# Performance work log

Measured on AMD Instinct MI355X. Metric: run time of the kernel, lower is better.

Reference implementation:

```python
import jax, jax.numpy as jnp
import numpy as np
from jax import lax

B, CIN, H, W = 2, 512, 64, 64
NCLS = 5
CI = CIN // 4      # inter_channels = 128
CQ = CI // 8       # PAM query/key channels = 16
EPS = 1e-5


def setup_inputs() -> dict:
    key = jax.random.key(0)
    it = iter(jax.random.split(key, 48))

    def nrm(shape, s=0.05):
        return jax.random.normal(next(it), shape, jnp.float32) * s

    def bn(c):
        w = jax.random.uniform(next(it), (c,), jnp.float32, 0.5, 1.5)
        b = nrm((c,))
        m = nrm((c,))
        v = jax.random.uniform(next(it), (c,), jnp.float32, 0.5, 1.5)
        return w, b, m, v

    inp = {}
    inp['x'] = jax.random.normal(next(it), (B, CIN, H, W), jnp.float32)
    inp['bn_a_w'], inp['bn_a_b'], inp['bn_a_m'], inp['bn_a_v'] = bn(CIN)
    inp['conv_a_w'] = nrm((CI, CIN, 3, 3))
    inp['bn_c_w'], inp['bn_c_b'], inp['bn_c_m'], inp['bn_c_v'] = bn(CIN)
    inp['conv_c_w'] = nrm((CI, CIN, 3, 3))
    inp['pam_q_w'] = nrm((CQ, CI)); inp['pam_q_b'] = nrm((CQ,))
    inp['pam_k_w'] = nrm((CQ, CI)); inp['pam_k_b'] = nrm((CQ,))
    inp['pam_v_w'] = nrm((CI, CI)); inp['pam_v_b'] = nrm((CI,))
    inp['pam_gamma'] = nrm((1,), 0.5)
    inp['cam_gamma'] = nrm((1,), 0.5)
    inp['bn_a1_w'], inp['bn_a1_b'], inp['bn_a1_m'], inp['bn_a1_v'] = bn(CI)
    inp['conv_a1_w'] = nrm((CIN, CI)); inp['conv_a1_b'] = nrm((CIN,))
    inp['bn_c1_w'], inp['bn_c1_b'], inp['bn_c1_m'], inp['bn_c1_v'] = bn(CI)
    inp['conv_c1_w'] = nrm((CIN, CI)); inp['conv_c1_b'] = nrm((CIN,))
    inp['out_a_w'] = nrm((NCLS, CIN)); inp['out_a_b'] = nrm((NCLS,))
    inp['out_c_w'] = nrm((NCLS, CIN)); inp['out_c_b'] = nrm((NCLS,))
    inp['out_f_w'] = nrm((NCLS, CIN)); inp['out_f_b'] = nrm((NCLS,))
    return inp


def _bn_relu(x, w, b, m, v):
    # eval-mode BatchNorm2d followed by ReLU
    scale = (w / jnp.sqrt(v + EPS))[None, :, None, None]
    shift = (b - m * w / jnp.sqrt(v + EPS))[None, :, None, None]
    return jax.nn.relu(x * scale + shift)


def _conv3(x, w):
    return lax.conv_general_dilated(x, w, (1, 1), 'SAME',
                                    dimension_numbers=('NCHW', 'OIHW', 'NCHW'))


def _conv1(x, w, b):
    # 1x1 conv as channel matmul
    return jnp.einsum('oi,bihw->bohw', w, x) + b[None, :, None, None]


def _pam(x, wq, bq, wk, bk, wv, bv, gamma):
    Bc, C, Hh, Ww = x.shape
    N = Hh * Ww
    q = _conv1(x, wq, bq).reshape(Bc, -1, N)   # [B,CQ,N]
    k = _conv1(x, wk, bk).reshape(Bc, -1, N)   # [B,CQ,N]
    v = _conv1(x, wv, bv).reshape(Bc, C, N)    # [B,C,N]
    energy = jnp.einsum('bcn,bcm->bnm', q, k)  # [B,N,N]
    attn = jax.nn.softmax(energy, axis=-1)
    out = jnp.einsum('bcm,bnm->bcn', v, attn).reshape(Bc, C, Hh, Ww)
    return gamma * out + x


def _cam(x, gamma):
    Bc, C, Hh, Ww = x.shape
    N = Hh * Ww
    f = x.reshape(Bc, C, N)
    energy = jnp.einsum('bcn,bdn->bcd', f, f)                    # [B,C,C]
    energy_new = jnp.max(energy, -1, keepdims=True) - energy
    attn = jax.nn.softmax(energy_new, axis=-1)
    out = jnp.einsum('bcd,bdn->bcn', attn, f).reshape(Bc, C, Hh, Ww)
    return gamma * out + x


def reference(x, bn_a_w, bn_a_b, bn_a_m, bn_a_v, conv_a_w,
              bn_c_w, bn_c_b, bn_c_m, bn_c_v, conv_c_w,
              pam_q_w, pam_q_b, pam_k_w, pam_k_b, pam_v_w, pam_v_b,
              pam_gamma, cam_gamma,
              bn_a1_w, bn_a1_b, bn_a1_m, bn_a1_v, conv_a1_w, conv_a1_b,
              bn_c1_w, bn_c1_b, bn_c1_m, bn_c1_v, conv_c1_w, conv_c1_b,
              out_a_w, out_a_b, out_c_w, out_c_b, out_f_w, out_f_b):
    # position-attention branch
    sa = _conv3(_bn_relu(x, bn_a_w, bn_a_b, bn_a_m, bn_a_v), conv_a_w)
    sa = _pam(sa, pam_q_w, pam_q_b, pam_k_w, pam_k_b, pam_v_w, pam_v_b, pam_gamma)
    sa = _conv1(_bn_relu(sa, bn_a1_w, bn_a1_b, bn_a1_m, bn_a1_v), conv_a1_w, conv_a1_b)
    # channel-attention branch
    sc = _conv3(_bn_relu(x, bn_c_w, bn_c_b, bn_c_m, bn_c_v), conv_c_w)
    sc = _cam(sc, cam_gamma)
    sc = _conv1(_bn_relu(sc, bn_c1_w, bn_c1_b, bn_c1_m, bn_c1_v), conv_c1_w, conv_c1_b)
    feat_fusion = sa + sc
    # dropout is identity at eval time
    sa_out = _conv1(sa, out_a_w, out_a_b)
    sc_out = _conv1(sc, out_c_w, out_c_b)
    sasc_out = _conv1(feat_fusion, out_f_w, out_f_b)
    return (feat_fusion, sasc_out, sa_out, sc_out)
```

## Files before the change

kernel.cpp:

```cpp
#include <hip/hip_runtime.h>

using u16 = unsigned short;
using short8 = __attribute__((ext_vector_type(8))) short;
using f32x4 = __attribute__((ext_vector_type(4))) float;

struct alignas(8) U16x4 { u16 x, y, z, w; };

__device__ __forceinline__ float bf2f(u16 u) {
  return __uint_as_float(((unsigned int)u) << 16);
}
__device__ __forceinline__ u16 f2bf(float f) {
  unsigned int u = __float_as_uint(f);
  unsigned int r = u + 0x7FFFu + ((u >> 16) & 1u);
  return (u16)(r >> 16);
}

__global__ void k_prep_w(const float* __restrict__ wa, const float* __restrict__ wc,
                         u16* __restrict__ Wb) {
  int idx = blockIdx.x * 256 + threadIdx.x;
  int j = idx & 7;
  int l = (idx >> 3) & 63;
  int ks = (idx >> 9) & 3;
  int rest = idx >> 11;
  int tap = rest % 9;
  int rest2 = rest / 9;
  int chunk = rest2 & 3;
  int mt = (rest2 >> 2) & 7;
  int br = rest2 >> 5;
  int co = mt * 16 + (l & 15);
  int ci = chunk * 128 + ks * 32 + (l >> 4) * 8 + j;
  const float* w = br ? wc : wa;
  Wb[idx] = f2bf(w[co * 4608 + ci * 9 + tap]);
}

__global__ void k_prep_w1(const float* __restrict__ wa, const float* __restrict__ wc,
                          u16* __restrict__ W1b) {
  int idx = blockIdx.x * 256 + threadIdx.x;
  int j = idx & 7;
  int l = (idx >> 3) & 63;
  int ks = (idx >> 9) & 3;
  int cot = (idx >> 11) & 31;
  int br = idx >> 16;
  int co = cot * 16 + (l & 15);
  int ci = ks * 32 + (l >> 4) * 8 + j;
  const float* w = br ? wc : wa;
  W1b[idx] = f2bf(w[co * 128 + ci]);
}

__global__ void k_prep_wqkv(const float* __restrict__ wq, const float* __restrict__ wk,
                            const float* __restrict__ wv, u16* __restrict__ Wq) {
  int idx = blockIdx.x * 256 + threadIdx.x;
  if (idx >= 20480) return;
  int j = idx & 7;
  int l = (idx >> 3) & 63;
  int ks = (idx >> 9) & 3;
  int cot = idx >> 11;
  int co = cot * 16 + (l & 15);
  int ci = ks * 32 + (l >> 4) * 8 + j;
  float w = co < 16 ? wq[co * 128 + ci]
          : (co < 32 ? wk[(co - 16) * 128 + ci] : wv[(co - 32) * 128 + ci]);
  Wq[idx] = f2bf(w);
}

__global__ __launch_bounds__(256) void k_bnrelu2t(const float* __restrict__ x,
    const float* __restrict__ wa, const float* __restrict__ ba,
    const float* __restrict__ ma, const float* __restrict__ va,
    const float* __restrict__ wc, const float* __restrict__ bc,
    const float* __restrict__ mc, const float* __restrict__ vc,
    u16* __restrict__ xa16, u16* __restrict__ xcb16) {
  __shared__ float sA[512], bA[512], sC[512], bC[512];
  __shared__ u16 ta[64 * 136], tc[64 * 136];
  int t = threadIdx.x;
  int h = blockIdx.x, b = blockIdx.y;
  for (int c = t; c < 512; c += 256) {
    float s1 = wa[c] * rsqrtf(va[c] + 1e-5f);
    sA[c] = s1; bA[c] = ba[c] - ma[c] * s1;
    float s2 = wc[c] * rsqrtf(vc[c] + 1e-5f);
    sC[c] = s2; bC[c] = bc[c] - mc[c] * s2;
  }
  __syncthreads();
  const float* xb = x + ((size_t)b << 21) + (h << 6);
  u16* oa = xa16 + ((size_t)b << 21) + ((size_t)h << 15);
  u16* oc = xcb16 + ((size_t)b << 21) + ((size_t)h << 15);
  int w = t & 63, cg = t >> 6;
  for (int c0 = 0; c0 < 512; c0 += 128) {
#pragma unroll
    for (int i = 0; i < 8; ++i) {
      int cl = cg * 4 + i * 16;
      int c = c0 + cl;
      const float* xp = xb + (size_t)c * 4096 + w;
      float v0 = xp[0], v1 = xp[4096], v2 = xp[8192], v3 = xp[12288];
      U16x4 pa, pc;
      pa.x = f2bf(fmaxf(fmaf(v0, sA[c], bA[c]), 0.f));
      pa.y = f2bf(fmaxf(fmaf(v1, sA[c + 1], bA[c + 1]), 0.f));
      pa.z = f2bf(fmaxf(fmaf(v2, sA[c + 2], bA[c + 2]), 0.f));
      pa.w = f2bf(fmaxf(fmaf(v3, sA[c + 3], bA[c + 3]), 0.f));
      pc.x = f2bf(fmaxf(fmaf(v0, sC[c], bC[c]), 0.f));
      pc.y = f2bf(fmaxf(fmaf(v1, sC[c + 1], bC[c + 1]), 0.f));
      pc.z = f2bf(fmaxf(fmaf(v2, sC[c + 2], bC[c + 2]), 0.f));
      pc.w = f2bf(fmaxf(fmaf(v3, sC[c + 3], bC[c + 3]), 0.f));
      *(U16x4*)(ta + w * 136 + cl) = pa;
      *(U16x4*)(tc + w * 136 + cl) = pc;
    }
    __syncthreads();
#pragma unroll
    for (int i = 0; i < 4; ++i) {
      int idx = t + i * 256;
      int ww = idx >> 4, c8 = (idx & 15) << 3;
      *(short8*)(oa + (size_t)ww * 512 + c0 + c8) = *(const short8*)(ta + ww * 136 + c8);
      *(short8*)(oc + (size_t)ww * 512 + c0 + c8) = *(const short8*)(tc + ww * 136 + c8);
    }
    __syncthreads();
  }
}

__global__ __launch_bounds__(256, 2) void k_conv3n(
    const u16* __restrict__ xa16, const u16* __restrict__ xcb16,
    const u16* __restrict__ Wb,
    float* __restrict__ sa0, float* __restrict__ sc0,
    u16* __restrict__ sa_nhwc, u16* __restrict__ sc16h, u16* __restrict__ sc16l) {
  __shared__ u16 xs[3 * 66 * 136];
  int t = threadIdx.x;
  int h = blockIdx.x;
  int z = blockIdx.y; int b = z & 1, br = z >> 1;
  int cosplit = blockIdx.z;
  const u16* xb = (br ? xcb16 : xa16) + ((size_t)b << 21);
  const u16* wb = Wb + (size_t)br * 589824;
  float* out = (br ? sc0 : sa0) + (((size_t)b * 128) << 12) + (h << 6);

  int lane = t & 63, wave = t >> 6;
  int mi = lane & 15, quad = lane >> 4;
  int mt = cosplit * 4 + wave;

  if (t < 96) {
    int dh = t >> 5, side = (t >> 4) & 1, c8 = t & 15;
    short8 z8 = {0, 0, 0, 0, 0, 0, 0, 0};
    *(short8*)(xs + (dh * 66 + side * 65) * 136 + c8 * 8) = z8;
  }

  f32x4 acc[4] = {};

  const u16* wlane = wb + lane * 8;
  const u16* bbase0 = xs + mi * 136 + quad * 8;

  for (int chunk = 0; chunk < 4; ++chunk) {
    int ci0 = chunk << 7;
    __syncthreads();
#pragma unroll
    for (int dh = 0; dh < 3; ++dh) {
      int hh = h + dh - 1;
      bool val = (hh >= 0) && (hh < 64);
      const u16* src = xb + (((size_t)hh << 6) << 9) + ci0;
#pragma unroll
      for (int i = 0; i < 4; ++i) {
        int idx = t + i * 256;
        int w = idx >> 4, c8 = (idx & 15) << 3;
        short8 v = {0, 0, 0, 0, 0, 0, 0, 0};
        if (val) v = *(const short8*)(src + ((size_t)w << 9) + c8);
        *(short8*)(xs + (dh * 66 + 1 + w) * 136 + c8) = v;
      }
    }
    __syncthreads();
    const u16* wchunk = wlane + (size_t)(mt * 4 + chunk) * 18432;
    short8 wreg[2][4];
#pragma unroll
    for (int ks = 0; ks < 4; ++ks)
      wreg[0][ks] = *(const short8*)(wchunk + ks * 512);
#pragma unroll
    for (int tap = 0; tap < 9; ++tap) {
      const int cb = tap & 1;
      if (tap < 8) {
        const u16* wn = wchunk + (tap + 1) * 2048;
#pragma unroll
        for (int ks = 0; ks < 4; ++ks)
          wreg[cb ^ 1][ks] = *(const short8*)(wn + ks * 512);
      }
      const int dh = tap / 3, dw = tap % 3;
      const u16* bp = bbase0 + (dh * 66 + dw) * 136;
#pragma unroll
      for (int ks = 0; ks < 4; ++ks) {
        short8 a = wreg[cb][ks];
#pragma unroll
        for (int nt = 0; nt < 4; ++nt) {
          short8 bf = *(const short8*)(bp + nt * 2176 + ks * 32);
          acc[nt] = __builtin_amdgcn_mfma_f32_16x16x32_bf16(a, bf, acc[nt], 0, 0, 0);
        }
      }
    }
  }
#pragma unroll
  for (int nt = 0; nt < 4; ++nt)
#pragma unroll
    for (int r = 0; r < 4; ++r) {
      int co = mt * 16 + quad * 4 + r;
      out[((size_t)co << 12) + nt * 16 + mi] = acc[nt][r];
    }
  if (br == 0) {
    u16* dstq = sa_nhwc + ((size_t)b << 19) + ((size_t)h << 6) * 128;
#pragma unroll
    for (int nt = 0; nt < 4; ++nt) {
      U16x4 v4;
      v4.x = f2bf(acc[nt][0]); v4.y = f2bf(acc[nt][1]);
      v4.z = f2bf(acc[nt][2]); v4.w = f2bf(acc[nt][3]);
      *(U16x4*)(dstq + (size_t)(nt * 16 + mi) * 128 + mt * 16 + quad * 4) = v4;
    }
  } else {
    u16* dh_ = sc16h + ((size_t)b << 19) + (h << 6);
    u16* dl_ = sc16l + ((size_t)b << 19) + (h << 6);
#pragma unroll
    for (int nt = 0; nt < 4; ++nt)
#pragma unroll
      for (int r = 0; r < 4; ++r) {
        int co = mt * 16 + quad * 4 + r;
        float xv = acc[nt][r];
        u16 hi = f2bf(xv);
        float lo = xv - bf2f(hi);
        size_t o = ((size_t)co << 12) + nt * 16 + mi;
        dh_[o] = hi;
        dl_[o] = f2bf(lo);
      }
  }
}

__global__ __launch_bounds__(256) void k_qkv(
    const u16* __restrict__ sa_nhwc, const u16* __restrict__ Wqkvb,
    const float* __restrict__ bq, const float* __restrict__ bk,
    const float* __restrict__ bv,
    float* __restrict__ qb, u16* __restrict__ k16t, u16* __restrict__ vt16) {
  __shared__ float bs[160];
  int t = threadIdx.x;
  int b = blockIdx.y, n0 = blockIdx.x * 128;
  if (t < 160) bs[t] = t < 16 ? bq[t] : (t < 32 ? bk[t - 16] : bv[t - 32]);
  __syncthreads();
  int lane = t & 63, wave = t >> 6;
  int mi = lane & 15, quad = lane >> 4;
  const u16* xb = sa_nhwc + ((size_t)b << 19) + (size_t)n0 * 128;
  const u16* wb = Wqkvb + lane * 8;
  f32x4 acc[2][10] = {};
  short8 bf[2][4];
#pragma unroll
  for (int ns = 0; ns < 2; ++ns) {
    int n = wave * 32 + ns * 16 + mi;
#pragma unroll
    for (int ks = 0; ks < 4; ++ks)
      bf[ns][ks] = *(const short8*)(xb + (size_t)n * 128 + ks * 32 + quad * 8);
  }
#pragma unroll
  for (int cot = 0; cot < 10; ++cot) {
    short8 a0 = *(const short8*)(wb + (size_t)(cot * 4 + 0) * 512);
    short8 a1 = *(const short8*)(wb + (size_t)(cot * 4 + 1) * 512);
    short8 a2 = *(const short8*)(wb + (size_t)(cot * 4 + 2) * 512);
    short8 a3 = *(const short8*)(wb + (size_t)(cot * 4 + 3) * 512);
#pragma unroll
    for (int ns = 0; ns < 2; ++ns) {
      acc[ns][cot] = __builtin_amdgcn_mfma_f32_16x16x32_bf16(a0, bf[ns][0], acc[ns][cot], 0, 0, 0);
      acc[ns][cot] = __builtin_amdgcn_mfma_f32_16x16x32_bf16(a1, bf[ns][1], acc[ns][cot], 0, 0, 0);
      acc[ns][cot] = __builtin_amdgcn_mfma_f32_16x16x32_bf16(a2, bf[ns][2], acc[ns][cot], 0, 0, 0);
      acc[ns][cot] = __builtin_amdgcn_mfma_f32_16x16x32_bf16(a3, bf[ns][3], acc[ns][cot], 0, 0, 0);
    }
  }
#pragma unroll
  for (int cot = 0; cot < 10; ++cot)
#pragma unroll
    for (int ns = 0; ns < 2; ++ns) {
      int n = n0 + wave * 32 + ns * 16 + mi;
      if (cot == 1) {
        u16 hv[4], lv[4];
#pragma unroll
        for (int r = 0; r < 4; ++r) {
          float v = acc[ns][1][r] + bs[16 + quad * 4 + r];
          u16 hi = f2bf(v);
          hv[r] = hi;
          lv[r] = f2bf(v - bf2f(hi));
        }
        u16* kd = k16t + (((size_t)b << 12) + n) * 32;
        U16x4 h4{hv[0], hv[1], hv[2], hv[3]};
        U16x4 l4{lv[0], lv[1], lv[2], lv[3]};
        *(U16x4*)(kd + quad * 4) = h4;
        *(U16x4*)(kd + 16 + quad * 4) = l4;
      } else {
#pragma unroll
        for (int r = 0; r < 4; ++r) {
          int co = cot * 16 + quad * 4 + r;
          float v = acc[ns][cot][r] + bs[co];
          if (co < 16) qb[((b * 16 + co) << 12) + n] = v;
          else vt16[((size_t)(b * 128 + co - 32) << 12) + n] = f2bf(v);
        }
      }
    }
}

__global__ __launch_bounds__(512, 4) void k_pam_pv(const float* __restrict__ qb,
    const u16* __restrict__ k16t, const u16* __restrict__ vt16,
    float* __restrict__ pvpart, float* __restrict__ pmax, float* __restrict__ psum) {
  constexpr int PSTR = 264;
  __shared__ u16 pL[32 * PSTR];
  __shared__ u16 qfh[32 * 16], qfl[32 * 16];
  __shared__ float wmx[8][2][16];
  __shared__ float wsm[8][2][16];
  int t = threadIdx.x;
  int b = blockIdx.y, n0 = blockIdx.x * 32;
  int mbeg = blockIdx.z << 11;
  int lane = t & 63, wave = t >> 6;
  int mi = lane & 15, quad = lane >> 4;
  int c0 = wave * 16;
  {
    int ch = t & 15, nl = t >> 4;
    float qv = qb[((size_t)(b * 16 + ch) << 12) + n0 + nl];
    u16 hi = f2bf(qv);
    qfh[nl * 16 + ch] = hi;
    qfl[nl * 16 + ch] = f2bf(qv - bf2f(hi));
  }
  const u16* kp = k16t + (((size_t)b << 12) + mbeg) * 32;
  const u16* vb = vt16 + ((size_t)b * 128 << 12);
  f32x4 acc[2] = {};
  float mr0 = -1e30f, mr1 = -1e30f, ssum0 = 0.f, ssum1 = 0.f;
  __syncthreads();
  int qoff = (quad & 1) * 8;
  short8 bq1[2], bq2[2];
  bq1[0] = *(const short8*)(qfh + mi * 16 + qoff);
  bq1[1] = *(const short8*)(qfh + (16 + mi) * 16 + qoff);
  bq2[0] = *(const short8*)(qfl + mi * 16 + qoff);
  bq2[1] = *(const short8*)(qfl + (16 + mi) * 16 + qoff);
  size_t abase = (size_t)(wave * 32 + mi) * 32 + quad * 8;
  short8 a0c = *(const short8*)(kp + abase);
  short8 a1c = *(const short8*)(kp + abase + 512);
  for (int it = 0; it < 8; ++it) {
    int m0r = it << 8;
    short8 vreg[8];
#pragma unroll
    for (int ksl = 0; ksl < 8; ++ksl)
      vreg[ksl] = *(const short8*)(vb + ((size_t)(c0 + mi) << 12) + mbeg + m0r + ksl * 32 + quad * 8);
    short8 a0n, a1n;
    if (it < 7) {
      a0n = *(const short8*)(kp + (size_t)(it + 1) * 8192 + abase);
      a1n = *(const short8*)(kp + (size_t)(it + 1) * 8192 + abase + 512);
    }
    f32x4 e00 = {}, e01 = {}, e10 = {}, e11 = {};
    e00 = __builtin_amdgcn_mfma_f32_16x16x32_bf16(a0c, bq1[0], e00, 0, 0, 0);
    e00 = __builtin_amdgcn_mfma_f32_16x16x32_bf16(a0c, bq2[0], e00, 0, 0, 0);
    e01 = __builtin_amdgcn_mfma_f32_16x16x32_bf16(a0c, bq1[1], e01, 0, 0, 0);
    e01 = __builtin_amdgcn_mfma_f32_16x16x32_bf16(a0c, bq2[1], e01, 0, 0, 0);
    e10 = __builtin_amdgcn_mfma_f32_16x16x32_bf16(a1c, bq1[0], e10, 0, 0, 0);
    e10 = __builtin_amdgcn_mfma_f32_16x16x32_bf16(a1c, bq2[0], e10, 0, 0, 0);
    e11 = __builtin_amdgcn_mfma_f32_16x16x32_bf16(a1c, bq1[1], e11, 0, 0, 0);
    e11 = __builtin_amdgcn_mfma_f32_16x16x32_bf16(a1c, bq2[1], e11, 0, 0, 0);
    float lm0 = fmaxf(fmaxf(fmaxf(e00[0], e00[1]), fmaxf(e00[2], e00[3])),
                      fmaxf(fmaxf(e10[0], e10[1]), fmaxf(e10[2], e10[3])));
    float lm1 = fmaxf(fmaxf(fmaxf(e01[0], e01[1]), fmaxf(e01[2], e01[3])),
                      fmaxf(fmaxf(e11[0], e11[1]), fmaxf(e11[2], e11[3])));
    lm0 = fmaxf(lm0, __shfl_xor(lm0, 16)); lm0 = fmaxf(lm0, __shfl_xor(lm0, 32));
    lm1 = fmaxf(lm1, __shfl_xor(lm1, 16)); lm1 = fmaxf(lm1, __shfl_xor(lm1, 32));
    if (quad == 0) { wmx[wave][0][mi] = lm0; wmx[wave][1][mi] = lm1; }
    __syncthreads();
    float cm0 = wmx[0][0][mi], cm1 = wmx[0][1][mi];
#pragma unroll
    for (int w = 1; w < 8; ++w) {
      cm0 = fmaxf(cm0, wmx[w][0][mi]);
      cm1 = fmaxf(cm1, wmx[w][1][mi]);
    }
    float mn0 = fmaxf(mr0, cm0), mn1 = fmaxf(mr1, cm1);
    float rs0 = __expf(mr0 - mn0), rs1 = __expf(mr1 - mn1);
#pragma unroll
    for (int r = 0; r < 4; ++r) { acc[0][r] *= rs0; acc[1][r] *= rs1; }
    float p00[4], p10[4], p01[4], p11[4];
    float ls0 = 0.f, ls1 = 0.f;
#pragma unroll
    for (int j = 0; j < 4; ++j) {
      p00[j] = __expf(e00[j] - mn0); p10[j] = __expf(e10[j] - mn0);
      p01[j] = __expf(e01[j] - mn1); p11[j] = __expf(e11[j] - mn1);
      ls0 += p00[j] + p10[j];
      ls1 += p01[j] + p11[j];
    }
    ssum0 = ssum0 * rs0 + ls0;
    ssum1 = ssum1 * rs1 + ls1;
    mr0 = mn0; mr1 = mn1;
    u16* prow0 = pL + mi * PSTR + wave * 32 + quad * 4;
    u16* prow1 = pL + (16 + mi) * PSTR + wave * 32 + quad * 4;
    U16x4 p;
    p.x = f2bf(p00[0]); p.y = f2bf(p00[1]); p.z = f2bf(p00[2]); p.w = f2bf(p00[3]);
    *(U16x4*)(prow0) = p;
    p.x = f2bf(p10[0]); p.y = f2bf(p10[1]); p.z = f2bf(p10[2]); p.w = f2bf(p10[3]);
    *(U16x4*)(prow0 + 16) = p;
    p.x = f2bf(p01[0]); p.y = f2bf(p01[1]); p.z = f2bf(p01[2]); p.w = f2bf(p01[3]);
    *(U16x4*)(prow1) = p;
    p.x = f2bf(p11[0]); p.y = f2bf(p11[1]); p.z = f2bf(p11[2]); p.w = f2bf(p11[3]);
    *(U16x4*)(prow1 + 16) = p;
    __syncthreads();
#pragma unroll
    for (int ksl = 0; ksl < 8; ++ksl) {
      const u16* pb0 = pL + mi * PSTR + ksl * 32 + quad * 8;
      short8 b0 = *(const short8*)(pb0);
      short8 b1 = *(const short8*)(pb0 + 16 * PSTR);
      acc[0] = __builtin_amdgcn_mfma_f32_16x16x32_bf16(vreg[ksl], b0, acc[0], 0, 0, 0);
      acc[1] = __builtin_amdgcn_mfma_f32_16x16x32_bf16(vreg[ksl], b1, acc[1], 0, 0, 0);
    }
    a0c = a0n; a1c = a1n;
  }
  ssum0 += __shfl_xor(ssum0, 16); ssum0 += __shfl_xor(ssum0, 32);
  ssum1 += __shfl_xor(ssum1, 16); ssum1 += __shfl_xor(ssum1, 32);
  if (quad == 0) { wsm[wave][0][mi] = ssum0; wsm[wave][1][mi] = ssum1; }
  __syncthreads();
  if (t < 16) {
    float sA = 0.f, sB = 0.f;
#pragma unroll
    for (int w = 0; w < 8; ++w) { sA += wsm[w][0][t]; sB += wsm[w][1][t]; }
    size_t base = ((size_t)(blockIdx.z * 2 + b) << 12) + n0;
    psum[base + t] = sA;
    psum[base + 16 + t] = sB;
    pmax[base + t] = mr0;
    pmax[base + 16 + t] = mr1;
  }
  float* dst = pvpart + (((size_t)(blockIdx.z * 2 + b) * 128) << 12);
#pragma unroll
  for (int nh = 0; nh < 2; ++nh)
#pragma unroll
    for (int r = 0; r < 4; ++r) {
      int c = c0 + quad * 4 + r;
      dst[((size_t)c << 12) + n0 + nh * 16 + mi] = acc[nh][r];
    }
}

__global__ __launch_bounds__(512) void k_cam_energy_m(
    const u16* __restrict__ sc16h, const u16* __restrict__ sc16l,
    float* __restrict__ epart) {
  int t = threadIdx.x;
  int ti = blockIdx.x, kc = blockIdx.y, b = blockIdx.z;
  int lane = t & 63, wave = t >> 6;
  int mi = lane & 15, quad = lane >> 4;
  const u16* fh = sc16h + ((size_t)b << 19);
  const u16* fl = sc16l + ((size_t)b << 19);
  size_t ao = ((size_t)(ti * 16 + mi) << 12) + (kc << 9) + quad * 8;
  size_t bo = ((size_t)(wave * 16 + mi) << 12) + (kc << 9) + quad * 8;
  const u16* ah = fh + ao; const u16* al = fl + ao;
  const u16* bh = fh + bo; const u16* bl = fl + bo;
  f32x4 acc = {};
#pragma unroll
  for (int k = 0; k < 16; ++k) {
    short8 vah = *(const short8*)(ah + k * 32);
    short8 val = *(const short8*)(al + k * 32);
    short8 vbh = *(const short8*)(bh + k * 32);
    short8 vbl = *(const short8*)(bl + k * 32);
    acc = __builtin_amdgcn_mfma_f32_16x16x32_bf16(vah, vbh, acc, 0, 0, 0);
    acc = __builtin_amdgcn_mfma_f32_16x16x32_bf16(vah, vbl, acc, 0, 0, 0);
    acc = __builtin_amdgcn_mfma_f32_16x16x32_bf16(val, vbh, acc, 0, 0, 0);
  }
  float* ep = epart + (((size_t)(kc * 2 + b)) << 14);
#pragma unroll
  for (int r = 0; r < 4; ++r)
    ep[((ti * 16 + quad * 4 + r) << 7) + wave * 16 + mi] = acc[r];
}

__global__ void k_cam_softmax(const float* __restrict__ epart, float* __restrict__ attn) {
  int lane = threadIdx.x;
  int c = blockIdx.x, b = blockIdx.y;
  float e0 = 0.f, e1 = 0.f;
#pragma unroll
  for (int kc = 0; kc < 8; ++kc) {
    const float* ep = epart + (((size_t)(kc * 2 + b)) << 14) + (c << 7);
    e0 += ep[lane];
    e1 += ep[lane + 64];
  }
  float mn = fminf(e0, e1);
#pragma unroll
  for (int off = 32; off >= 1; off >>= 1) mn = fminf(mn, __shfl_xor(mn, off));
  float p0 = __expf(fminf(mn - e0, 0.f)), p1 = __expf(fminf(mn - e1, 0.f));
  float s = p0 + p1;
#pragma unroll
  for (int off = 32; off >= 1; off >>= 1) s += __shfl_xor(s, off);
  float inv = 1.f / s;
  float* a = attn + ((b * 128 + c) << 7);
  a[lane] = p0 * inv;
  a[lane + 64] = p1 * inv;
}

__global__ __launch_bounds__(256) void k_cam_out(const float* __restrict__ f,
    const float* __restrict__ attn, const float* __restrict__ gamma,
    float* __restrict__ sc1) {
  __shared__ float at2[128 * 16];
  int t = threadIdx.x;
  int b = blockIdx.z, c0 = blockIdx.y * 16;
  int n = blockIdx.x * 256 + t;
  for (int idx = t; idx < 2048; idx += 256) {
    int d = idx >> 4, cc = idx & 15;
    at2[idx] = attn[((b * 128 + c0 + cc) << 7) + d];
  }
  __syncthreads();
  float acc[16] = {};
  const float* fb = f + ((size_t)b * 128 << 12) + n;
  for (int d = 0; d < 128; ++d) {
    float fv = fb[d << 12];
    const float* ap = at2 + d * 16;
#pragma unroll
    for (int cc = 0; cc < 16; ++cc) acc[cc] = fmaf(ap[cc], fv, acc[cc]);
  }
  float g = gamma[0];
#pragma unroll
  for (int cc = 0; cc < 16; ++cc) {
    size_t o = ((size_t)(b * 128 + c0 + cc) << 12) + n;
    sc1[o] = fmaf(g, acc[cc], f[o]);
  }
}

__global__ __launch_bounds__(256, 2) void k_bout_m(
    const float* __restrict__ sa0, const float* __restrict__ pvpart,
    const float* __restrict__ pmax, const float* __restrict__ psum,
    const float* __restrict__ gamma,
    const float* __restrict__ sc1,
    const float* __restrict__ wa_, const float* __restrict__ ba_,
    const float* __restrict__ ma_, const float* __restrict__ va_,
    const float* __restrict__ wc_, const float* __restrict__ bc_,
    const float* __restrict__ mc_, const float* __restrict__ vc_,
    const u16* __restrict__ W1b, const float* __restrict__ Ba,
    const float* __restrict__ Bc,
    u16* __restrict__ sa2, u16* __restrict__ sc2) {
  __shared__ u16 xl[32 * 136];
  __shared__ float scl[128], shf[128];
  int t = threadIdx.x;
  int n0 = blockIdx.x * 32;
  int b = blockIdx.y, br = blockIdx.z;
  const float* bw = br ? wc_ : wa_;
  const float* bb = br ? bc_ : ba_;
  const float* bm = br ? mc_ : ma_;
  const float* bvv = br ? vc_ : va_;
  if (t < 128) {
    float s = bw[t] * rsqrtf(bvv[t] + 1e-5f);
    scl[t] = s;
    shf[t] = bb[t] - bm[t] * s;
  }
  __syncthreads();
  {
    int nl = t & 31, cio = t >> 5;
    const float* s0 = (br ? sc1 : sa0) + ((size_t)b * 128 << 12) + n0 + nl;
    const float* p0 = pvpart + ((size_t)b * 128 << 12) + n0 + nl;
    const float* p1 = pvpart + (((size_t)(2 + b) * 128) << 12) + n0 + nl;
    float k0 = 0.f, k1 = 0.f;
    if (!br) {
      int n = n0 + nl;
      float m0 = pmax[((size_t)b << 12) + n];
      float m1 = pmax[((size_t)(2 + b) << 12) + n];
      float sA = psum[((size_t)b << 12) + n];
      float sB = psum[((size_t)(2 + b) << 12) + n];
      float M = fmaxf(m0, m1);
      float w0 = __expf(m0 - M), w1 = __expf(m1 - M);
      float inv = gamma[0] / (w0 * sA + w1 * sB);
      k0 = w0 * inv; k1 = w1 * inv;
    }
#pragma unroll
    for (int half = 0; half < 2; ++half) {
      short8 v;
#pragma unroll
      for (int i = 0; i < 8; ++i) {
        int ci = cio * 16 + half * 8 + i;
        float xv = s0[(size_t)ci << 12];
        if (!br) xv += k0 * p0[(size_t)ci << 12] + k1 * p1[(size_t)ci << 12];
        v[i] = (short)f2bf(fmaxf(fmaf(xv, scl[ci], shf[ci]), 0.f));
      }
      *(short8*)(xl + nl * 136 + cio * 16 + half * 8) = v;
    }
  }
  __syncthreads();
  int lane = t & 63, wave = t >> 6;
  int mi = lane & 15, quad = lane >> 4;
  const u16* wb = W1b + (size_t)br * 65536 + lane * 8;
  f32x4 acc[8][2] = {};
#pragma unroll
  for (int ks = 0; ks < 4; ++ks) {
    short8 b0 = *(const short8*)(xl + mi * 136 + ks * 32 + quad * 8);
    short8 b1 = *(const short8*)(xl + (16 + mi) * 136 + ks * 32 + quad * 8);
#pragma unroll
    for (int ct = 0; ct < 8; ++ct) {
      int cot = wave * 8 + ct;
      short8 a = *(const short8*)(wb + ((size_t)(cot * 4 + ks) << 9));
      acc[ct][0] = __builtin_amdgcn_mfma_f32_16x16x32_bf16(a, b0, acc[ct][0], 0, 0, 0);
      acc[ct][1] = __builtin_amdgcn_mfma_f32_16x16x32_bf16(a, b1, acc[ct][1], 0, 0, 0);
    }
  }
  const float* Bs = br ? Bc : Ba;
  u16* dst = br ? sc2 : sa2;
#pragma unroll
  for (int ct = 0; ct < 8; ++ct)
#pragma unroll
    for (int nh = 0; nh < 2; ++nh)
#pragma unroll
      for (int r = 0; r < 4; ++r) {
        int co = (wave * 8 + ct) * 16 + quad * 4 + r;
        dst[((size_t)(b * 512 + co) << 12) + n0 + nh * 16 + mi] =
            f2bf(acc[ct][nh][r] + Bs[co]);
      }
}

__global__ __launch_bounds__(256) void k_heads2(const u16* __restrict__ sa2,
    const u16* __restrict__ sc2,
    const float* __restrict__ wf, const float* __restrict__ wa, const float* __restrict__ wc,
    const float* __restrict__ bfb, const float* __restrict__ bab,
    const float* __restrict__ bcb,
    float* __restrict__ outFusion, float* __restrict__ outCls) {
  __shared__ float lw[3 * 5 * 512];
  __shared__ float hs[8][15][32];
  int t = threadIdx.x;
  int b = blockIdx.y, n0 = blockIdx.x * 32;
  for (int idx = t; idx < 7680; idx += 256) {
    int arr = idx / 2560, rest = idx - arr * 2560;
    int cls = rest >> 9, co = rest & 511;
    const float* w = arr == 0 ? wf : (arr == 1 ? wa : wc);
    lw[idx] = w[cls * 512 + co];
  }
  __syncthreads();
  int nl = t & 31, ck = t >> 5;
  float acc[15] = {};
  for (int co = ck * 64; co < ck * 64 + 64; ++co) {
    size_t o = ((size_t)(b * 512 + co) << 12) + n0 + nl;
    float a = bf2f(sa2[o]), c = bf2f(sc2[o]);
    float s = a + c;
    outFusion[o] = s;
    const float* lf = lw + co;
#pragma unroll
    for (int cls = 0; cls < 5; ++cls) {
      acc[cls]      = fmaf(lf[cls * 512], s, acc[cls]);
      acc[5 + cls]  = fmaf(lf[2560 + cls * 512], a, acc[5 + cls]);
      acc[10 + cls] = fmaf(lf[5120 + cls * 512], c, acc[10 + cls]);
    }
  }
#pragma unroll
  for (int k = 0; k < 15; ++k) hs[ck][k][nl] = acc[k];
  __syncthreads();
  for (int idx = t; idx < 480; idx += 256) {
    int k = idx >> 5, nl2 = idx & 31;
    float s = 0.f;
#pragma unroll
    for (int c8 = 0; c8 < 8; ++c8) s += hs[c8][k][nl2];
    int arr = k / 5, cls = k - arr * 5;
    float bias = arr == 0 ? bfb[cls] : (arr == 1 ? bab[cls] : bcb[cls]);
    outCls[arr * 40960 + ((b * 5 + cls) << 12) + n0 + nl2] = s + bias;
  }
}

extern "C" void kernel_launch(void* const* d_in, const int* in_sizes, int n_in,
                              void* d_out, int out_size, void* d_ws, size_t ws_size,
                              hipStream_t stream) {
  (void)in_sizes; (void)n_in; (void)out_size; (void)ws_size;
  const float* x      = (const float*)d_in[0];
  const float* bnaw   = (const float*)d_in[1];
  const float* bnab   = (const float*)d_in[2];
  const float* bnam   = (const float*)d_in[3];
  const float* bnav   = (const float*)d_in[4];
  const float* convaw = (const float*)d_in[5];
  const float* bncw   = (const float*)d_in[6];
  const float* bncb   = (const float*)d_in[7];
  const float* bncm   = (const float*)d_in[8];
  const float* bncv   = (const float*)d_in[9];
  const float* convcw = (const float*)d_in[10];
  const float* pqw    = (const float*)d_in[11];
  const float* pqb    = (const float*)d_in[12];
  const float* pkw    = (const float*)d_in[13];
  const float* pkb    = (const float*)d_in[14];
  const float* pvw    = (const float*)d_in[15];
  const float* pvb    = (const float*)d_in[16];
  const float* pgam   = (const float*)d_in[17];
  const float* cgam   = (const float*)d_in[18];
  const float* bna1w  = (const float*)d_in[19];
  const float* bna1b  = (const float*)d_in[20];
  const float* bna1m  = (const float*)d_in[21];
  const float* bna1v  = (const float*)d_in[22];
  const float* conva1w = (const float*)d_in[23];
  const float* conva1b = (const float*)d_in[24];
  const float* bnc1w  = (const float*)d_in[25];
  const float* bnc1b  = (const float*)d_in[26];
  const float* bnc1m  = (const float*)d_in[27];
  const float* bnc1v  = (const float*)d_in[28];
  const float* convc1w = (const float*)d_in[29];
  const float* convc1b = (const float*)d_in[30];
  const float* outaw  = (const float*)d_in[31];
  const float* outab  = (const float*)d_in[32];
  const float* outcw  = (const float*)d_in[33];
  const float* outcb  = (const float*)d_in[34];
  const float* outfw  = (const float*)d_in[35];
  const float* outfb  = (const float*)d_in[36];

  char* wsb = (char*)d_ws;
  size_t off = 0;
  auto take = [&](size_t bytes) -> void* {
    void* p = wsb + off;
    off += (bytes + 255) & ~(size_t)255;
    return p;
  };
  u16*   Wb    = (u16*)take((size_t)2 * 128 * 9 * 512 * 2);
  u16*   W1b   = (u16*)take((size_t)2 * 512 * 128 * 2);
  u16*   Wqkvb = (u16*)take((size_t)160 * 128 * 2);
  u16*   xa16  = (u16*)take((size_t)2 * 512 * 4096 * 2);
  u16*   xcb16 = (u16*)take((size_t)2 * 512 * 4096 * 2);
  float* sa0   = (float*)take((size_t)2 * 128 * 4096 * 4);
  float* sc0   = (float*)take((size_t)2 * 128 * 4096 * 4);
  u16*   sa_nhwc = (u16*)take((size_t)2 * 4096 * 128 * 2);
  u16*   sc16h = (u16*)take((size_t)2 * 128 * 4096 * 2);
  u16*   sc16l = (u16*)take((size_t)2 * 128 * 4096 * 2);
  float* qb    = (float*)take((size_t)2 * 16 * 4096 * 4);
  u16*   k16t  = (u16*)take((size_t)2 * 4096 * 32 * 2);
  u16*   vt16  = (u16*)take((size_t)2 * 128 * 4096 * 2);
  float* pvpart = (float*)take((size_t)2 * 2 * 128 * 4096 * 4);
  float* pmax  = (float*)take((size_t)2 * 2 * 4096 * 4);
  float* psum  = (float*)take((size_t)2 * 2 * 4096 * 4);
  float* sc1   = (float*)take((size_t)2 * 128 * 4096 * 4);
  float* epart = (float*)take((size_t)8 * 2 * 128 * 128 * 4);
  float* attn  = (float*)take((size_t)2 * 128 * 128 * 4);
  u16*   sa2   = (u16*)take((size_t)2 * 512 * 4096 * 2);
  u16*   sc2   = (u16*)take((size_t)2 * 512 * 4096 * 2);

  float* outF = (float*)d_out;
  float* outCls = outF + (size_t)2 * 512 * 4096;

  k_prep_w<<<4608, 256, 0, stream>>>(convaw, convcw, Wb);
  k_prep_w1<<<512, 256, 0, stream>>>(conva1w, convc1w, W1b);
  k_prep_wqkv<<<80, 256, 0, stream>>>(pqw, pkw, pvw, Wqkvb);
  k_bnrelu2t<<<dim3(64, 2), 256, 0, stream>>>(x, bnaw, bnab, bnam, bnav,
                                              bncw, bncb, bncm, bncv, xa16, xcb16);
  k_conv3n<<<dim3(64, 4, 2), 256, 0, stream>>>(xa16, xcb16, Wb, sa0, sc0,
                                               sa_nhwc, sc16h, sc16l);
  k_qkv<<<dim3(32, 2), 256, 0, stream>>>(sa_nhwc, Wqkvb, pqb, pkb, pvb,
                                         qb, k16t, vt16);
  k_pam_pv<<<dim3(128, 2, 2), 512, 0, stream>>>(qb, k16t, vt16, pvpart, pmax, psum);
  k_cam_energy_m<<<dim3(8, 8, 2), 512, 0, stream>>>(sc16h, sc16l, epart);
  k_cam_softmax<<<dim3(128, 2), 64, 0, stream>>>(epart, attn);
  k_cam_out<<<dim3(16, 8, 2), 256, 0, stream>>>(sc0, attn, cgam, sc1);
  k_bout_m<<<dim3(128, 2, 2), 256, 0, stream>>>(sa0, pvpart, pmax, psum, pgam, sc1,
      bna1w, bna1b, bna1m, bna1v, bnc1w, bnc1b, bnc1m, bnc1v,
      W1b, conva1b, convc1b, sa2, sc2);
  k_heads2<<<dim3(128, 2), 256, 0, stream>>>(sa2, sc2, outfw, outaw, outcw,
                                             outfb, outab, outcb, outF, outCls);
}
```

Measured before the change: 308.1 us.

## Increase grid parallelism across bnrelu, PAM split-K, CAM output and heads kernels

Splits several under-occupied kernels into more blocks. The bnrelu transpose now gets one block per 128-channel chunk, and PAM attention is split into four key ranges instead of two, with the merge kernel combining four partial softmax states. The CAM output and the heads kernel handle fewer channels or pixels per block. The goal is to fill more compute units on a GPU where these grids were small (128–512 blocks). In exchange there is more partial-result traffic (pvpart doubles in size), more merge arithmetic, and more redundant parameter loads per block.

```diff
diff --git a/kernel.cpp b/kernel.cpp
--- a/kernel.cpp
+++ b/kernel.cpp
@@ -68,49 +68,48 @@
     const float* __restrict__ wc, const float* __restrict__ bc,
     const float* __restrict__ mc, const float* __restrict__ vc,
     u16* __restrict__ xa16, u16* __restrict__ xcb16) {
-  __shared__ float sA[512], bA[512], sC[512], bC[512];
+  __shared__ float sA[128], bA[128], sC[128], bC[128];
   __shared__ u16 ta[64 * 136], tc[64 * 136];
   int t = threadIdx.x;
   int h = blockIdx.x, b = blockIdx.y;
-  for (int c = t; c < 512; c += 256) {
+  int c0 = blockIdx.z * 128;
+  if (t < 128) {
+    int c = c0 + t;
     float s1 = wa[c] * rsqrtf(va[c] + 1e-5f);
-    sA[c] = s1; bA[c] = ba[c] - ma[c] * s1;
+    sA[t] = s1; bA[t] = ba[c] - ma[c] * s1;
     float s2 = wc[c] * rsqrtf(vc[c] + 1e-5f);
-    sC[c] = s2; bC[c] = bc[c] - mc[c] * s2;
+    sC[t] = s2; bC[t] = bc[c] - mc[c] * s2;
   }
   __syncthreads();
   const float* xb = x + ((size_t)b << 21) + (h << 6);
   u16* oa = xa16 + ((size_t)b << 21) + ((size_t)h << 15);
   u16* oc = xcb16 + ((size_t)b << 21) + ((size_t)h << 15);
   int w = t & 63, cg = t >> 6;
-  for (int c0 = 0; c0 < 512; c0 += 128) {
-#pragma unroll
-    for (int i = 0; i < 8; ++i) {
-      int cl = cg * 4 + i * 16;
-      int c = c0 + cl;
-      const float* xp = xb + (size_t)c * 4096 + w;
-      float v0 = xp[0], v1 = xp[4096], v2 = xp[8192], v3 = xp[12288];
-      U16x4 pa, pc;
-      pa.x = f2bf(fmaxf(fmaf(v0, sA[c], bA[c]), 0.f));
-      pa.y = f2bf(fmaxf(fmaf(v1, sA[c + 1], bA[c + 1]), 0.f));
-      pa.z = f2bf(fmaxf(fmaf(v2, sA[c + 2], bA[c + 2]), 0.f));
-      pa.w = f2bf(fmaxf(fmaf(v3, sA[c + 3], bA[c + 3]), 0.f));
-      pc.x = f2bf(fmaxf(fmaf(v0, sC[c], bC[c]), 0.f));
-      pc.y = f2bf(fmaxf(fmaf(v1, sC[c + 1], bC[c + 1]), 0.f));
-      pc.z = f2bf(fmaxf(fmaf(v2, sC[c + 2], bC[c + 2]), 0.f));
-      pc.w = f2bf(fmaxf(fmaf(v3, sC[c + 3], bC[c + 3]), 0.f));
-      *(U16x4*)(ta + w * 136 + cl) = pa;
-      *(U16x4*)(tc + w * 136 + cl) = pc;
-    }
-    __syncthreads();
-#pragma unroll
-    for (int i = 0; i < 4; ++i) {
-      int idx = t + i * 256;
-      int ww = idx >> 4, c8 = (idx & 15) << 3;
-      *(short8*)(oa + (size_t)ww * 512 + c0 + c8) = *(const short8*)(ta + ww * 136 + c8);
-      *(short8*)(oc + (size_t)ww * 512 + c0 + c8) = *(const short8*)(tc + ww * 136 + c8);
-    }
-    __syncthreads();
+#pragma unroll
+  for (int i = 0; i < 8; ++i) {
+    int cl = cg * 4 + i * 16;
+    int c = c0 + cl;
+    const float* xp = xb + (size_t)c * 4096 + w;
+    float v0 = xp[0], v1 = xp[4096], v2 = xp[8192], v3 = xp[12288];
+    U16x4 pa, pc;
+    pa.x = f2bf(fmaxf(fmaf(v0, sA[cl], bA[cl]), 0.f));
+    pa.y = f2bf(fmaxf(fmaf(v1, sA[cl + 1], bA[cl + 1]), 0.f));
+    pa.z = f2bf(fmaxf(fmaf(v2, sA[cl + 2], bA[cl + 2]), 0.f));
+    pa.w = f2bf(fmaxf(fmaf(v3, sA[cl + 3], bA[cl + 3]), 0.f));
+    pc.x = f2bf(fmaxf(fmaf(v0, sC[cl], bC[cl]), 0.f));
+    pc.y = f2bf(fmaxf(fmaf(v1, sC[cl + 1], bC[cl + 1]), 0.f));
+    pc.z = f2bf(fmaxf(fmaf(v2, sC[cl + 2], bC[cl + 2]), 0.f));
+    pc.w = f2bf(fmaxf(fmaf(v3, sC[cl + 3], bC[cl + 3]), 0.f));
+    *(U16x4*)(ta + w * 136 + cl) = pa;
+    *(U16x4*)(tc + w * 136 + cl) = pc;
+  }
+  __syncthreads();
+#pragma unroll
+  for (int i = 0; i < 4; ++i) {
+    int idx = t + i * 256;
+    int ww = idx >> 4, c8 = (idx & 15) << 3;
+    *(short8*)(oa + (size_t)ww * 512 + c0 + c8) = *(const short8*)(ta + ww * 136 + c8);
+    *(short8*)(oc + (size_t)ww * 512 + c0 + c8) = *(const short8*)(tc + ww * 136 + c8);
   }
 }
 
@@ -300,7 +299,8 @@
   __shared__ float wsm[8][2][16];
   int t = threadIdx.x;
   int b = blockIdx.y, n0 = blockIdx.x * 32;
-  int mbeg = blockIdx.z << 11;
+  int mq = blockIdx.z;
+  int mbeg = mq << 10;
   int lane = t & 63, wave = t >> 6;
   int mi = lane & 15, quad = lane >> 4;
   int c0 = wave * 16;
@@ -325,14 +325,14 @@
   size_t abase = (size_t)(wave * 32 + mi) * 32 + quad * 8;
   short8 a0c = *(const short8*)(kp + abase);
   short8 a1c = *(const short8*)(kp + abase + 512);
-  for (int it = 0; it < 8; ++it) {
+  for (int it = 0; it < 4; ++it) {
     int m0r = it << 8;
     short8 vreg[8];
 #pragma unroll
     for (int ksl = 0; ksl < 8; ++ksl)
       vreg[ksl] = *(const short8*)(vb + ((size_t)(c0 + mi) << 12) + mbeg + m0r + ksl * 32 + quad * 8);
     short8 a0n, a1n;
-    if (it < 7) {
+    if (it < 3) {
       a0n = *(const short8*)(kp + (size_t)(it + 1) * 8192 + abase);
       a1n = *(const short8*)(kp + (size_t)(it + 1) * 8192 + abase + 512);
     }
@@ -405,13 +405,13 @@
     float sA = 0.f, sB = 0.f;
 #pragma unroll
     for (int w = 0; w < 8; ++w) { sA += wsm[w][0][t]; sB += wsm[w][1][t]; }
-    size_t base = ((size_t)(blockIdx.z * 2 + b) << 12) + n0;
+    size_t base = ((size_t)(mq * 2 + b) << 12) + n0;
     psum[base + t] = sA;
     psum[base + 16 + t] = sB;
     pmax[base + t] = mr0;
     pmax[base + 16 + t] = mr1;
   }
-  float* dst = pvpart + (((size_t)(blockIdx.z * 2 + b) * 128) << 12);
+  float* dst = pvpart + (((size_t)(mq * 2 + b) * 128) << 12);
 #pragma unroll
   for (int nh = 0; nh < 2; ++nh)
 #pragma unroll
@@ -477,26 +477,26 @@
 __global__ __launch_bounds__(256) void k_cam_out(const float* __restrict__ f,
     const float* __restrict__ attn, const float* __restrict__ gamma,
     float* __restrict__ sc1) {
-  __shared__ float at2[128 * 16];
+  __shared__ float at2[128 * 8];
   int t = threadIdx.x;
-  int b = blockIdx.z, c0 = blockIdx.y * 16;
+  int b = blockIdx.z, c0 = blockIdx.y * 8;
   int n = blockIdx.x * 256 + t;
-  for (int idx = t; idx < 2048; idx += 256) {
-    int d = idx >> 4, cc = idx & 15;
+  for (int idx = t; idx < 1024; idx += 256) {
+    int d = idx >> 3, cc = idx & 7;
     at2[idx] = attn[((b * 128 + c0 + cc) << 7) + d];
   }
   __syncthreads();
-  float acc[16] = {};
+  float acc[8] = {};
   const float* fb = f + ((size_t)b * 128 << 12) + n;
   for (int d = 0; d < 128; ++d) {
     float fv = fb[d << 12];
-    const float* ap = at2 + d * 16;
-#pragma unroll
-    for (int cc = 0; cc < 16; ++cc) acc[cc] = fmaf(ap[cc], fv, acc[cc]);
+    const float* ap = at2 + d * 8;
+#pragma unroll
+    for (int cc = 0; cc < 8; ++cc) acc[cc] = fmaf(ap[cc], fv, acc[cc]);
   }
   float g = gamma[0];
 #pragma unroll
-  for (int cc = 0; cc < 16; ++cc) {
+  for (int cc = 0; cc < 8; ++cc) {
     size_t o = ((size_t)(b * 128 + c0 + cc) << 12) + n;
     sc1[o] = fmaf(g, acc[cc], f[o]);
   }
@@ -532,19 +532,24 @@
   {
     int nl = t & 31, cio = t >> 5;
     const float* s0 = (br ? sc1 : sa0) + ((size_t)b * 128 << 12) + n0 + nl;
-    const float* p0 = pvpart + ((size_t)b * 128 << 12) + n0 + nl;
-    const float* p1 = pvpart + (((size_t)(2 + b) * 128) << 12) + n0 + nl;
-    float k0 = 0.f, k1 = 0.f;
+    const float* pq[4];
+    float kq[4] = {};
     if (!br) {
       int n = n0 + nl;
-      float m0 = pmax[((size_t)b << 12) + n];
-      float m1 = pmax[((size_t)(2 + b) << 12) + n];
-      float sA = psum[((size_t)b << 12) + n];
-      float sB = psum[((size_t)(2 + b) << 12) + n];
-      float M = fmaxf(m0, m1);
-      float w0 = __expf(m0 - M), w1 = __expf(m1 - M);
-      float inv = gamma[0] / (w0 * sA + w1 * sB);
-      k0 = w0 * inv; k1 = w1 * inv;
+      float m[4], s4[4];
+#pragma unroll
+      for (int q = 0; q < 4; ++q) {
+        pq[q] = pvpart + (((size_t)(q * 2 + b) * 128) << 12) + n0 + nl;
+        m[q] = pmax[((size_t)(q * 2 + b) << 12) + n];
+        s4[q] = psum[((size_t)(q * 2 + b) << 12) + n];
+      }
+      float M = fmaxf(fmaxf(m[0], m[1]), fmaxf(m[2], m[3]));
+      float den = 0.f;
+#pragma unroll
+      for (int q = 0; q < 4; ++q) { kq[q] = __expf(m[q] - M); den = fmaf(kq[q], s4[q], den); }
+      float inv = gamma[0] / den;
+#pragma unroll
+      for (int q = 0; q < 4; ++q) kq[q] *= inv;
     }
 #pragma unroll
     for (int half = 0; half < 2; ++half) {
@@ -553,7 +558,11 @@
       for (int i = 0; i < 8; ++i) {
         int ci = cio * 16 + half * 8 + i;
         float xv = s0[(size_t)ci << 12];
-        if (!br) xv += k0 * p0[(size_t)ci << 12] + k1 * p1[(size_t)ci << 12];
+        if (!br) {
+          size_t po = (size_t)ci << 12;
+          xv += kq[0] * pq[0][po] + kq[1] * pq[1][po]
+              + kq[2] * pq[2][po] + kq[3] * pq[3][po];
+        }
         v[i] = (short)f2bf(fmaxf(fmaf(xv, scl[ci], shf[ci]), 0.f));
       }
       *(short8*)(xl + nl * 136 + cio * 16 + half * 8) = v;
@@ -597,9 +606,9 @@
     const float* __restrict__ bcb,
     float* __restrict__ outFusion, float* __restrict__ outCls) {
   __shared__ float lw[3 * 5 * 512];
-  __shared__ float hs[8][15][32];
+  __shared__ float hs[16][15][16];
   int t = threadIdx.x;
-  int b = blockIdx.y, n0 = blockIdx.x * 32;
+  int b = blockIdx.y, n0 = blockIdx.x * 16;
   for (int idx = t; idx < 7680; idx += 256) {
     int arr = idx / 2560, rest = idx - arr * 2560;
     int cls = rest >> 9, co = rest & 511;
@@ -607,9 +616,9 @@
     lw[idx] = w[cls * 512 + co];
   }
   __syncthreads();
-  int nl = t & 31, ck = t >> 5;
+  int nl = t & 15, ck = t >> 4;
   float acc[15] = {};
-  for (int co = ck * 64; co < ck * 64 + 64; ++co) {
+  for (int co = ck * 32; co < ck * 32 + 32; ++co) {
     size_t o = ((size_t)(b * 512 + co) << 12) + n0 + nl;
     float a = bf2f(sa2[o]), c = bf2f(sc2[o]);
     float s = a + c;
@@ -625,11 +634,11 @@
 #pragma unroll
   for (int k = 0; k < 15; ++k) hs[ck][k][nl] = acc[k];
   __syncthreads();
-  for (int idx = t; idx < 480; idx += 256) {
-    int k = idx >> 5, nl2 = idx & 31;
+  for (int idx = t; idx < 240; idx += 256) {
+    int k = idx >> 4, nl2 = idx & 15;
     float s = 0.f;
 #pragma unroll
-    for (int c8 = 0; c8 < 8; ++c8) s += hs[c8][k][nl2];
+    for (int c8 = 0; c8 < 16; ++c8) s += hs[c8][k][nl2];
     int arr = k / 5, cls = k - arr * 5;
     float bias = arr == 0 ? bfb[cls] : (arr == 1 ? bab[cls] : bcb[cls]);
     outCls[arr * 40960 + ((b * 5 + cls) << 12) + n0 + nl2] = s + bias;
@@ -698,9 +707,9 @@
   float* qb    = (float*)take((size_t)2 * 16 * 4096 * 4);
   u16*   k16t  = (u16*)take((size_t)2 * 4096 * 32 * 2);
   u16*   vt16  = (u16*)take((size_t)2 * 128 * 4096 * 2);
-  float* pvpart = (float*)take((size_t)2 * 2 * 128 * 4096 * 4);
-  float* pmax  = (float*)take((size_t)2 * 2 * 4096 * 4);
-  float* psum  = (float*)take((size_t)2 * 2 * 4096 * 4);
+  float* pvpart = (float*)take((size_t)4 * 2 * 128 * 4096 * 4);
+  float* pmax  = (float*)take((size_t)4 * 2 * 4096 * 4);
+  float* psum  = (float*)take((size_t)4 * 2 * 4096 * 4);
   float* sc1   = (float*)take((size_t)2 * 128 * 4096 * 4);
   float* epart = (float*)take((size_t)8 * 2 * 128 * 128 * 4);
   float* attn  = (float*)take((size_t)2 * 128 * 128 * 4);
@@ -713,19 +722,19 @@
   k_prep_w<<<4608, 256, 0, stream>>>(convaw, convcw, Wb);
   k_prep_w1<<<512, 256, 0, stream>>>(conva1w, convc1w, W1b);
   k_prep_wqkv<<<80, 256, 0, stream>>>(pqw, pkw, pvw, Wqkvb);
-  k_bnrelu2t<<<dim3(64, 2), 256, 0, stream>>>(x, bnaw, bnab, bnam, bnav,
-                                              bncw, bncb, bncm, bncv, xa16, xcb16);
+  k_bnrelu2t<<<dim3(64, 2, 4), 256, 0, stream>>>(x, bnaw, bnab, bnam, bnav,
+                                                 bncw, bncb, bncm, bncv, xa16, xcb16);
   k_conv3n<<<dim3(64, 4, 2), 256, 0, stream>>>(xa16, xcb16, Wb, sa0, sc0,
                                                sa_nhwc, sc16h, sc16l);
   k_qkv<<<dim3(32, 2), 256, 0, stream>>>(sa_nhwc, Wqkvb, pqb, pkb, pvb,
                                          qb, k16t, vt16);
-  k_pam_pv<<<dim3(128, 2, 2), 512, 0, stream>>>(qb, k16t, vt16, pvpart, pmax, psum);
+  k_pam_pv<<<dim3(128, 2, 4), 512, 0, stream>>>(qb, k16t, vt16, pvpart, pmax, psum);
   k_cam_energy_m<<<dim3(8, 8, 2), 512, 0, stream>>>(sc16h, sc16l, epart);
   k_cam_softmax<<<dim3(128, 2), 64, 0, stream>>>(epart, attn);
-  k_cam_out<<<dim3(16, 8, 2), 256, 0, stream>>>(sc0, attn, cgam, sc1);
+  k_cam_out<<<dim3(16, 16, 2), 256, 0, stream>>>(sc0, attn, cgam, sc1);
   k_bout_m<<<dim3(128, 2, 2), 256, 0, stream>>>(sa0, pvpart, pmax, psum, pgam, sc1,
       bna1w, bna1b, bna1m, bna1v, bnc1w, bnc1b, bnc1m, bnc1v,
       W1b, conva1b, convc1b, sa2, sc2);
-  k_heads2<<<dim3(128, 2), 256, 0, stream>>>(sa2, sc2, outfw, outaw, outcw,
+  k_heads2<<<dim3(256, 2), 256, 0, stream>>>(sa2, sc2, outfw, outaw, outcw,
                                              outfb, outab, outcb, outF, outCls);
 }
```

Measured after the change: 292.3 us (median of 2 runs). 5.1% less time.
